# Performance work log

Measured on AMD Instinct MI355X. Metric: run time of the kernel, lower is better.

Reference implementation:

```python
import jax, jax.numpy as jnp
import numpy as np


def setup_inputs() -> dict:
    key = jax.random.key(0)
    k1, k2, k3, k4, k5 = jax.random.split(key, 5)
    B, T, nu, nx, ny = 32, 4096, 64, 128, 64
    return {
        "u_": jax.random.normal(k1, (B, T, nu), dtype=jnp.float32),
        "M": jax.random.normal(k2, (2 * nx, 2 * nx), dtype=jnp.float32),
        "B_mat": jax.random.normal(k3, (nx, nu), dtype=jnp.float32),
        "C": jax.random.normal(k4, (ny, nx), dtype=jnp.float32),
        "x0": jax.random.normal(k5, (nx,), dtype=jnp.float32),
    }


def reference(u_, M, B_mat, C, x0):
    # LMI-stable A parameterization: S = M M^T + tol*I,
    # F = S[nx:, :nx], P = S[nx:, nx:], E = 0.5*(P + S[:nx, :nx]), A = E^{-1} F
    nx = x0.shape[0]
    tol_A = 1e-9
    S = M @ M.T + tol_A * jnp.eye(2 * nx, dtype=M.dtype)
    Fm = S[nx:, :nx]
    E = 0.5 * (S[nx:, nx:] + S[:nx, :nx])
    A = jnp.linalg.solve(E, Fm)  # == inv(E) @ Fm

    Bsz = u_.shape[0]
    x_init = jnp.broadcast_to(x0, (Bsz, nx))  # learned x0 tiled over batch

    # x_{t+1} = A x_t + B u_t ; y_t = C x_t ; y_0 = C x_0
    def step(x, u_t):
        x_new = x @ A.T + u_t @ B_mat.T  # [B, nx]
        return x_new, x_new @ C.T        # emit y_{t+1} [B, ny]

    u_tm = jnp.swapaxes(u_[:, :-1, :], 0, 1)  # [T-1, B, nu] (u[T-1] unused)
    _, ys = jax.lax.scan(step, x_init, u_tm)   # [T-1, B, ny]

    y0 = (x_init @ C.T)[:, None, :]            # [B, 1, ny]
    return jnp.concatenate([y0, jnp.swapaxes(ys, 0, 1)], axis=1)  # [B, T, ny]
```

## Files before the change

### kernel.cpp

```cpp
#include <hip/hip_runtime.h>

#define BATCH 32
#define T_LEN 4096
#define NU 64
#define NX 128
#define NY 64
#define KCH 64
#define NC (T_LEN / KCH)
#define KSPLIT 8

#define OFF_E    0
#define OFF_F    16384
#define OFF_A    32768
#define OFF_G    49152
#define OFF_A8   81920
#define OFF_A16  98304
#define OFF_A32  114688
#define OFF_A64  131072
#define OFF_D    147456
#define OFF_P    204800
#define OFF_WT   233472
#define OFF_WF   380928
#define OFF_WBH  905216
#define OFF_WBL  1167360
#define OFF_XC   1429504
#define OFF_L    1691648
#define OFF_V8   1953792
#define OFF_X8   4050944
#define OFF_UBH  5099520
#define OFF_UBL  9293824
#define OFF_LP   13488128
#define WS_NEED_FLOATS (13488128 + 2097152)

__device__ __forceinline__ int XP(int l)   { return l + ((l >> 3) << 2); }
__device__ __forceinline__ int UP16(int l) { return l + ((l >> 4) << 2); }

__device__ __forceinline__ unsigned short f2bf(float f) {
    unsigned int x = __float_as_uint(f);
    unsigned int r = (x + 0x7FFFu + ((x >> 16) & 1u)) >> 16;
    return (unsigned short)r;
}
__device__ __forceinline__ float bf2f(unsigned short h) {
    return __uint_as_float(((unsigned int)h) << 16);
}
__device__ __forceinline__ float4 f4ms(float4 a, float s, float4 b) {
    float4 r;
    r.x = a.x - s * b.x; r.y = a.y - s * b.y;
    r.z = a.z - s * b.z; r.w = a.w - s * b.w;
    return r;
}
__device__ __forceinline__ float f4dot(float4 a, float4 b) {
    return a.x * b.x + a.y * b.y + a.z * b.z + a.w * b.w;
}
__device__ __forceinline__ void cvt_one(const float* __restrict__ src,
                                        unsigned short* __restrict__ hi,
                                        unsigned short* __restrict__ lo,
                                        size_t idx) {
    float4 v = ((const float4*)src)[idx];
    unsigned short h0 = f2bf(v.x), h1 = f2bf(v.y), h2 = f2bf(v.z), h3 = f2bf(v.w);
    unsigned short l0 = f2bf(v.x - bf2f(h0));
    unsigned short l1 = f2bf(v.y - bf2f(h1));
    unsigned short l2 = f2bf(v.z - bf2f(h2));
    unsigned short l3 = f2bf(v.w - bf2f(h3));
    unsigned long long ph = (unsigned long long)h0 | ((unsigned long long)h1 << 16)
                          | ((unsigned long long)h2 << 32) | ((unsigned long long)h3 << 48);
    unsigned long long pl = (unsigned long long)l0 | ((unsigned long long)l1 << 16)
                          | ((unsigned long long)l2 << 32) | ((unsigned long long)l3 << 48);
    ((unsigned long long*)hi)[idx] = ph;
    ((unsigned long long*)lo)[idx] = pl;
}

typedef __attribute__((ext_vector_type(8))) short bf16x8;
typedef __attribute__((ext_vector_type(4))) float f32x4;

__global__ __launch_bounds__(256) void efcvt_kernel(const float* __restrict__ M,
                                                    float* __restrict__ E,
                                                    float* __restrict__ F,
                                                    const float* __restrict__ u,
                                                    unsigned short* __restrict__ hi,
                                                    unsigned short* __restrict__ lo,
                                                    int n4) {
    int blk = blockIdx.x;
    if (blk < 256) {
        int part = blk >> 7;
        int i = blk & 127;
        int j = threadIdx.x;
        if (j < 128) {
            const float* Mi2 = M + (size_t)(128 + i) * 256;
            const float* Mj1 = M + (size_t)j * 256;
            if (part == 0) {
                const float* Mi1 = M + (size_t)i * 256;
                const float* Mj2 = M + (size_t)(128 + j) * 256;
                float s11 = 0.f, s22 = 0.f;
                for (int m = 0; m < 256; ++m) {
                    s11 += Mi1[m] * Mj1[m];
                    s22 += Mi2[m] * Mj2[m];
                }
                float e = 0.5f * (s11 + s22);
                if (i == j) e += 1e-9f;
                E[i * NX + j] = e;
            } else {
                float s21 = 0.f;
                for (int m = 0; m < 256; ++m) s21 += Mi2[m] * Mj1[m];
                F[i * NX + j] = s21;
            }
        }
    } else if (hi != nullptr) {
        size_t stride = (size_t)(gridDim.x - 256) * 256;
        for (size_t idx = (size_t)(blk - 256) * 256 + threadIdx.x; idx < (size_t)n4;
             idx += stride)
            cvt_one(u, hi, lo, idx);
    }
}

__global__ __launch_bounds__(512, 1) void solve_kernel(const float* __restrict__ E,
                                                       const float* __restrict__ F,
                                                       float* __restrict__ A) {
    __shared__ __align__(16) float praw[2][4][264];
    __shared__ __align__(16) float4 mrowS[2][128];
    __shared__ float pivarr[128];
    int t = threadIdx.x;
    int rg = t >> 4, seg = t & 15;

    float4 R[4][4];
#pragma unroll
    for (int k = 0; k < 4; ++k) {
        int r = rg + 32 * k;
        const float4* erow = (const float4*)(E + (size_t)r * NX);
        const float4* frow = (const float4*)(F + (size_t)r * NX);
        R[k][0] = erow[seg];
        R[k][1] = erow[seg + 16];
        R[k][2] = frow[seg];
        R[k][3] = frow[seg + 16];
    }
    if (rg < 4) {
        float4* dst = (float4*)&praw[0][rg][0];
        dst[seg]      = R[0][0];
        dst[seg + 16] = R[0][1];
        dst[seg + 32] = R[0][2];
        dst[seg + 48] = R[0][3];
    }
    if (seg == 0) {
#pragma unroll
        for (int k = 0; k < 4; ++k) mrowS[0][rg + 32 * k] = R[k][0];
    }
    __syncthreads();

    int buf = 0;
    for (int wd = 0; wd < 32; ++wd) {
        int k0 = 4 * wd;
        const float* p0s = &praw[buf][0][0];
        const float* p1s = &praw[buf][1][0];
        const float* p2s = &praw[buf][2][0];
        const float* p3s = &praw[buf][3][0];
        float p00 = p0s[k0], p01 = p0s[k0 + 1], p02 = p0s[k0 + 2], p03 = p0s[k0 + 3];
        float r10 = p1s[k0], r11 = p1s[k0 + 1], r12 = p1s[k0 + 2], r13 = p1s[k0 + 3];
        float r20 = p2s[k0], r21 = p2s[k0 + 1], r22 = p2s[k0 + 2], r23 = p2s[k0 + 3];
        float r30 = p3s[k0], r31 = p3s[k0 + 1], r32 = p3s[k0 + 2], r33 = p3s[k0 + 3];
        float inv0 = 1.0f / p00;
        float m1 = r10 * inv0;
        float piv1 = r11 - m1 * p01;
        float inv1 = 1.0f / piv1;
        float p12 = r12 - m1 * p02, p13 = r13 - m1 * p03;
        float m2 = r20 * inv0;
        float m2b = (r21 - m2 * p01) * inv1;
        float piv2 = r22 - m2 * p02 - m2b * p12;
        float inv2 = 1.0f / piv2;
        float p23 = r23 - m2 * p03 - m2b * p13;
        float m3 = r30 * inv0;
        float m3b = (r31 - m3 * p01) * inv1;
        float m3c = (r32 - m3 * p02 - m3b * p12) * inv2;
        float piv3 = r33 - m3 * p03 - m3b * p13 - m3c * p23;
        float inv3 = 1.0f / piv3;
        if (t == 0) {
            pivarr[k0] = p00; pivarr[k0 + 1] = piv1;
            pivarr[k0 + 2] = piv2; pivarr[k0 + 3] = piv3;
        }
        float q0[4], q1[4], q2[4], q3[4];
#pragma unroll
        for (int k = 0; k < 4; ++k) {
            int r = rg + 32 * k;
            float4 mv = mrowS[buf][r];
            int d = r - k0;
            float a = mv.x * inv0;
            if (d == 0) a = 0.f;
            float b2 = (mv.y - a * p01) * inv1;
            if (d == 1) b2 = 0.f;
            float c2 = (mv.z - a * p02 - b2 * p12) * inv2;
            if (d == 2) c2 = 0.f;
            float e2 = (mv.w - a * p03 - b2 * p13 - c2 * p23) * inv3;
            if (d == 3) e2 = 0.f;
            q0[k] = a; q1[k] = b2; q2[k] = c2; q3[k] = e2;
        }
        const float4* w0 = (const float4*)&praw[buf][0][0];
        const float4* w1 = (const float4*)&praw[buf][1][0];
        const float4* w2 = (const float4*)&praw[buf][2][0];
        const float4* w3 = (const float4*)&praw[buf][3][0];
#pragma unroll
        for (int j = 0; j < 4; ++j) {
            int g = seg + 16 * j;
            float4 a0 = w0[g], a1 = w1[g], a2 = w2[g], a3 = w3[g];
            float4 p1v = f4ms(a1, m1, a0);
            float4 p2v = f4ms(f4ms(a2, m2, a0), m2b, p1v);
            float4 p3v = f4ms(f4ms(f4ms(a3, m3, a0), m3b, p1v), m3c, p2v);
#pragma unroll
            for (int k = 0; k < 4; ++k) {
                float4 acc = R[k][j];
                acc = f4ms(acc, q0[k], a0);
                acc = f4ms(acc, q1[k], p1v);
                acc = f4ms(acc, q2[k], p2v);
                acc = f4ms(acc, q3[k], p3v);
                R[k][j] = acc;
            }
        }
        if (wd < 31) {
#pragma unroll
            for (int k = 0; k < 4; ++k) {
                int r = rg + 32 * k;
                int d2 = r - (k0 + 4);
                if (d2 >= 0 && d2 < 4) {
                    float4* dst = (float4*)&praw[buf ^ 1][d2][0];
                    dst[seg]      = R[k][0];
                    dst[seg + 16] = R[k][1];
                    dst[seg + 32] = R[k][2];
                    dst[seg + 48] = R[k][3];
                }
            }
            if (seg == ((wd + 1) & 15)) {
#pragma unroll
                for (int k = 0; k < 4; ++k) {
                    float4 sel = ((wd + 1) < 16) ? R[k][0] : R[k][1];
                    mrowS[buf ^ 1][rg + 32 * k] = sel;
                }
            }
        }
        __syncthreads();
        buf ^= 1;
    }

#pragma unroll
    for (int k = 0; k < 4; ++k) {
        int r = rg + 32 * k;
        float s = 1.0f / pivarr[r];
        float4* dst = (float4*)(A + (size_t)r * NX);
        float4 v2 = R[k][2];
        v2.x *= s; v2.y *= s; v2.z *= s; v2.w *= s;
        dst[seg] = v2;
        float4 v3 = R[k][3];
        v3.x *= s; v3.y *= s; v3.z *= s; v3.w *= s;
        dst[seg + 16] = v3;
    }
}

struct MMDesc { const float* X; const float* Y; float* Z; int N; int ldX; int ldY; int ldZ; int Mrows; };
struct MMB { MMDesc d[4]; };
__global__ __launch_bounds__(128) void mmb_kernel(MMB mm) {
    MMDesc d = mm.d[blockIdx.y];
    if (d.Z == nullptr) return;
    int nct = (d.N + 127) >> 7;
    int i = blockIdx.x / nct;
    int jt = blockIdx.x - i * nct;
    if (i >= d.Mrows) return;
    int j = jt * 128 + threadIdx.x;
    if (j >= d.N) return;
    if (d.Y == nullptr) {
        d.Z[(size_t)i * d.ldZ + j] = d.X[(size_t)i * d.ldX + j];
        return;
    }
    const float* xr = d.X + (size_t)i * d.ldX;
    float a0 = 0.f, a1 = 0.f, a2 = 0.f, a3 = 0.f;
    for (int m = 0; m < 128; m += 4) {
        a0 += xr[m]     * d.Y[(size_t)(m)     * d.ldY + j];
        a1 += xr[m + 1] * d.Y[(size_t)(m + 1) * d.ldY + j];
        a2 += xr[m + 2] * d.Y[(size_t)(m + 2) * d.ldY + j];
        a3 += xr[m + 3] * d.Y[(size_t)(m + 3) * d.ldY + j];
    }
    d.Z[(size_t)i * d.ldZ + j] = (a0 + a1) + (a2 + a3);
}

__global__ __launch_bounds__(576) void wcvt_kernel(const float* __restrict__ Dm,
                                                   const float* __restrict__ C,
                                                   const float* __restrict__ Pm,
                                                   unsigned short* __restrict__ WT,
                                                   const float* __restrict__ WF,
                                                   unsigned short* __restrict__ WBH,
                                                   unsigned short* __restrict__ WBL,
                                                   int n4) {
    int blk = blockIdx.x;
    if (blk < 512) {
        int o = blk;
        int f = threadIdx.x;
        int k = o >> 6, yi = o & 63;
        float v = 0.f;
        if (f < 128) {
            v = (k == 0) ? C[(size_t)yi * NX + f]
                         : Dm[(size_t)(k - 1) * 64 * NX + (size_t)yi * NX + f];
        } else {
            int j = (f - 128) >> 6, e = (f - 128) & 63;
            if (k > j) v = Pm[(size_t)(k - 1 - j) * 64 * 64 + (size_t)yi * 64 + e];
        }
        WT[(size_t)o * 576 + f] = f2bf(v);
    } else {
        size_t idx = (size_t)(blk - 512) * 576 + threadIdx.x;
        if (idx < (size_t)n4) cvt_one(WF, WBH, WBL, idx);
    }
}

__global__ __launch_bounds__(256) void lvgemm_kernel(const unsigned short* __restrict__ UH,
                                                     const unsigned short* __restrict__ UL,
                                                     const unsigned short* __restrict__ WH,
                                                     const unsigned short* __restrict__ WL,
                                                     float* __restrict__ Lp,
                                                     float* __restrict__ V8) {
    int t = threadIdx.x;
    int w = t >> 6, l = t & 63;
    int l16 = l & 15, l4 = l >> 4;
    int o0 = w * 32 + l16;
    f32x4 acc[4][2];
#pragma unroll
    for (int mt = 0; mt < 4; ++mt)
#pragma unroll
        for (int nt = 0; nt < 2; ++nt) acc[mt][nt] = (f32x4){0.f, 0.f, 0.f, 0.f};

    if (blockIdx.x < 256) {
        int blk = blockIdx.x & 31;
        int kblk = blockIdx.x >> 5;
        size_t uoff[4];
#pragma unroll
        for (int mt = 0; mt < 4; ++mt) {
            int pair = blk * 64 + mt * 16 + l16;
            int b = pair & 31, c = pair >> 5;
            uoff[mt] = ((size_t)b * T_LEN + (size_t)c * KCH) * NU;
        }
        int kt0 = kblk * (128 / KSPLIT);
        for (int kt = kt0; kt < kt0 + 128 / KSPLIT; ++kt) {
            int feat = kt * 32 + l4 * 8;
            bf16x8 ah[4], al[4], bh[2], bl[2];
#pragma unroll
            for (int mt = 0; mt < 4; ++mt) {
                ah[mt] = *(const bf16x8*)(UH + uoff[mt] + feat);
                al[mt] = *(const bf16x8*)(UL + uoff[mt] + feat);
            }
#pragma unroll
            for (int nt = 0; nt < 2; ++nt) {
                size_t woff = (size_t)(o0 + nt * 16) * 4096 + feat;
                bh[nt] = *(const bf16x8*)(WH + woff);
                bl[nt] = *(const bf16x8*)(WL + woff);
            }
#pragma unroll
            for (int mt = 0; mt < 4; ++mt)
#pragma unroll
                for (int nt = 0; nt < 2; ++nt) {
                    acc[mt][nt] = __builtin_amdgcn_mfma_f32_16x16x32_bf16(
                        ah[mt], bh[nt], acc[mt][nt], 0, 0, 0);
                    acc[mt][nt] = __builtin_amdgcn_mfma_f32_16x16x32_bf16(
                        ah[mt], bl[nt], acc[mt][nt], 0, 0, 0);
                    acc[mt][nt] = __builtin_amdgcn_mfma_f32_16x16x32_bf16(
                        al[mt], bh[nt], acc[mt][nt], 0, 0, 0);
                }
        }
        float* lout = Lp + (size_t)kblk * 2048 * NX;
#pragma unroll
        for (int mt = 0; mt < 4; ++mt)
#pragma unroll
            for (int nt = 0; nt < 2; ++nt)
#pragma unroll
                for (int reg = 0; reg < 4; ++reg) {
                    int r = blk * 64 + mt * 16 + l4 * 4 + reg;
                    lout[(size_t)r * NX + o0 + nt * 16] = acc[mt][nt][reg];
                }
    } else {
        int blk = blockIdx.x - 256;
        size_t uoff[4];
#pragma unroll
        for (int mt = 0; mt < 4; ++mt) {
            int r = blk * 64 + mt * 16 + l16;
            int pair = r >> 3, q = r & 7;
            int b = pair & 31, c = pair >> 5;
            uoff[mt] = ((size_t)b * T_LEN + (size_t)c * KCH + (size_t)q * 8) * NU;
        }
#pragma unroll 2
        for (int kt = 0; kt < 16; ++kt) {
            int feat = kt * 32 + l4 * 8;
            bf16x8 ah[4], al[4], bh[2], bl[2];
#pragma unroll
            for (int mt = 0; mt < 4; ++mt) {
                ah[mt] = *(const bf16x8*)(UH + uoff[mt] + feat);
                al[mt] = *(const bf16x8*)(UL + uoff[mt] + feat);
            }
#pragma unroll
            for (int nt = 0; nt < 2; ++nt) {
                size_t woff = (size_t)(o0 + nt * 16) * 4096 + 3584 + feat;
                bh[nt] = *(const bf16x8*)(WH + woff);
                bl[nt] = *(const bf16x8*)(WL + woff);
            }
#pragma unroll
            for (int mt = 0; mt < 4; ++mt)
#pragma unroll
                for (int nt = 0; nt < 2; ++nt) {
                    acc[mt][nt] = __builtin_amdgcn_mfma_f32_16x16x32_bf16(
                        ah[mt], bh[nt], acc[mt][nt], 0, 0, 0);
                    acc[mt][nt] = __builtin_amdgcn_mfma_f32_16x16x32_bf16(
                        ah[mt], bl[nt], acc[mt][nt], 0, 0, 0);
                    acc[mt][nt] = __builtin_amdgcn_mfma_f32_16x16x32_bf16(
                        al[mt], bh[nt], acc[mt][nt], 0, 0, 0);
                }
        }
#pragma unroll
        for (int mt = 0; mt < 4; ++mt)
#pragma unroll
            for (int nt = 0; nt < 2; ++nt)
#pragma unroll
                for (int reg = 0; reg < 4; ++reg) {
                    int r = blk * 64 + mt * 16 + l4 * 4 + reg;
                    V8[(size_t)r * NX + o0 + nt * 16] = acc[mt][nt][reg];
                }
    }
}

__global__ __launch_bounds__(128) void phase2_kernel(const float* __restrict__ AK,
                                                     const float* __restrict__ Lp,
                                                     const float* __restrict__ x0,
                                                     float* __restrict__ Xc) {
    __shared__ float Ks[NX][NX + 1];
    __shared__ float xs[NX];
    int tid = threadIdx.x, b = blockIdx.x;
    for (int idx = tid; idx < NX * NX; idx += 128)
        Ks[idx >> 7][idx & 127] = AK[idx];
    float x = x0[tid];
    xs[tid] = x;
    Xc[(size_t)(0 * BATCH + b) * NX + tid] = x;
    __syncthreads();
    for (int c = 0; c < NC - 1; ++c) {
        size_t lidx = ((size_t)c * BATCH + b) * NX + tid;
        float lsum = 0.f;
#pragma unroll
        for (int k = 0; k < KSPLIT; ++k) lsum += Lp[(size_t)k * 2048 * NX + lidx];
        float a0 = 0.f, a1 = 0.f, a2 = 0.f, a3 = 0.f;
        for (int j = 0; j < NX; j += 4) {
            a0 += Ks[tid][j]     * xs[j];
            a1 += Ks[tid][j + 1] * xs[j + 1];
            a2 += Ks[tid][j + 2] * xs[j + 2];
            a3 += Ks[tid][j + 3] * xs[j + 3];
        }
        float xn = (a0 + a1) + (a2 + a3) + lsum;
        __syncthreads();
        xs[tid] = xn;
        Xc[((size_t)(c + 1) * BATCH + b) * NX + tid] = xn;
        __syncthreads();
    }
}

__global__ __launch_bounds__(128) void phase2fb_kernel(const float* __restrict__ AK,
                                                       const float* __restrict__ L,
                                                       const float* __restrict__ x0,
                                                       float* __restrict__ Xc) {
    __shared__ float Ks[NX][NX + 1];
    __shared__ float xs[NX];
    int tid = threadIdx.x, b = blockIdx.x;
    for (int idx = tid; idx < NX * NX; idx += 128)
        Ks[idx >> 7][idx & 127] = AK[idx];
    float x = x0[tid];
    xs[tid] = x;
    Xc[(size_t)(0 * BATCH + b) * NX + tid] = x;
    __syncthreads();
    for (int c = 0; c < NC - 1; ++c) {
        float a0 = 0.f, a1 = 0.f, a2 = 0.f, a3 = 0.f;
        for (int j = 0; j < NX; j += 4) {
            a0 += Ks[tid][j]     * xs[j];
            a1 += Ks[tid][j + 1] * xs[j + 1];
            a2 += Ks[tid][j + 2] * xs[j + 2];
            a3 += Ks[tid][j + 3] * xs[j + 3];
        }
        float xn = (a0 + a1) + (a2 + a3) + L[((size_t)c * BATCH + b) * NX + tid];
        __syncthreads();
        xs[tid] = xn;
        Xc[((size_t)(c + 1) * BATCH + b) * NX + tid] = xn;
        __syncthreads();
    }
}

__global__ __launch_bounds__(256, 4) void chain8_kernel(const float* __restrict__ A8,
                                                        const float* __restrict__ V8,
                                                        const float* __restrict__ Xc,
                                                        unsigned short* __restrict__ X8) {
    int t = threadIdx.x;
    int g = t >> 3, seg = t & 7;
    int pair = blockIdx.x;

    float4 A8r[4][4];
#pragma unroll
    for (int r = 0; r < 4; ++r) {
        const float4* ap = (const float4*)(A8 + (size_t)(g + 32 * r) * NX + seg * 16);
        A8r[r][0] = ap[0]; A8r[r][1] = ap[1]; A8r[r][2] = ap[2]; A8r[r][3] = ap[3];
    }

    __shared__ __align__(16) float xs[2][192];
    __shared__ float vs[2][128];
    float vreg = 0.f;
    if (t < NX) {
        xs[0][XP(t)] = Xc[(size_t)pair * NX + t];
        vreg = V8[((size_t)pair * 8) * NX + t];
    }

    int buf = 0;
    for (int m = 0; m < 8; ++m) {
        if (t < NX) vs[buf][t] = vreg;
        if (t < NX && m < 7) vreg = V8[((size_t)pair * 8 + m + 1) * NX + t];
        __syncthreads();
        if (t < NX) X8[((size_t)pair * 8 + m) * NX + t] = f2bf(xs[buf][XP(t)]);
        const float4* xq0 = (const float4*)&xs[buf][seg * 24];
        const float4* xq1 = (const float4*)&xs[buf][seg * 24 + 12];
        float4 x0 = xq0[0], x1 = xq0[1], x2 = xq1[0], x3 = xq1[1];
        float acc[4];
#pragma unroll
        for (int r = 0; r < 4; ++r) {
            acc[r] = (f4dot(A8r[r][0], x0) + f4dot(A8r[r][1], x1))
                   + (f4dot(A8r[r][2], x2) + f4dot(A8r[r][3], x3));
        }
#pragma unroll
        for (int d = 1; d <= 4; d <<= 1) {
#pragma unroll
            for (int r = 0; r < 4; ++r) acc[r] += __shfl_xor(acc[r], d);
        }
        if (seg == 0) {
            xs[buf ^ 1][XP(g)]      = acc[0] + vs[buf][g];
            xs[buf ^ 1][XP(g + 32)] = acc[1] + vs[buf][g + 32];
            xs[buf ^ 1][XP(g + 64)] = acc[2] + vs[buf][g + 64];
            xs[buf ^ 1][XP(g + 96)] = acc[3] + vs[buf][g + 96];
        }
        buf ^= 1;
    }
}

__global__ __launch_bounds__(512) void yemit_mfma_kernel(const unsigned short* __restrict__ X8,
                                                         const unsigned short* __restrict__ ub,
                                                         const unsigned short* __restrict__ WT,
                                                         float* __restrict__ y) {
    int t = threadIdx.x;
    int w = t >> 6, l = t & 63;
    int l16 = l & 15, l4 = l >> 4;
    int blk = blockIdx.x;
    f32x4 acc[4][4];
#pragma unroll
    for (int mt = 0; mt < 4; ++mt)
#pragma unroll
        for (int nt = 0; nt < 4; ++nt) acc[mt][nt] = (f32x4){0.f, 0.f, 0.f, 0.f};
    int grow[4];
    const unsigned short* ubase[4];
#pragma unroll
    for (int mt = 0; mt < 4; ++mt) {
        grow[mt] = blk * 64 + mt * 16 + l16;
        int pair = grow[mt] >> 3, q = grow[mt] & 7;
        int b = pair & 31, cc = pair >> 5;
        ubase[mt] = ub + ((size_t)b * T_LEN + (size_t)cc * KCH + (size_t)q * 8) * NU;
    }
#pragma unroll 2
    for (int kt = 0; kt < 18; ++kt) {
        int feat = kt * 32 + l4 * 8;
        bf16x8 afr[4];
#pragma unroll
        for (int mt = 0; mt < 4; ++mt) {
            const unsigned short* ap;
            if (feat < 128) ap = X8 + (size_t)grow[mt] * NX + feat;
            else            ap = ubase[mt] + (feat - 128);
            afr[mt] = *(const bf16x8*)ap;
        }
        bf16x8 bfr[4];
#pragma unroll
        for (int nt = 0; nt < 4; ++nt) {
            int o = w * 64 + nt * 16 + l16;
            bfr[nt] = *(const bf16x8*)(WT + (size_t)o * 576 + feat);
        }
#pragma unroll
        for (int mt = 0; mt < 4; ++mt)
#pragma unroll
            for (int nt = 0; nt < 4; ++nt)
                acc[mt][nt] = __builtin_amdgcn_mfma_f32_16x16x32_bf16(
                    afr[mt], bfr[nt], acc[mt][nt], 0, 0, 0);
    }
#pragma unroll
    for (int mt = 0; mt < 4; ++mt) {
#pragma unroll
        for (int nt = 0; nt < 4; ++nt) {
            int o = w * 64 + nt * 16 + l16;
            int k = o >> 6, yi = o & 63;
#pragma unroll
            for (int reg = 0; reg < 4; ++reg) {
                int r = blk * 64 + mt * 16 + l4 * 4 + reg;
                int pair = r >> 3, q = r & 7;
                int b = pair & 31, cc = pair >> 5;
                int tt = cc * KCH + q * 8 + k;
                y[((size_t)b * T_LEN + tt) * NY + yi] = acc[mt][nt][reg];
            }
        }
    }
}

__global__ __launch_bounds__(512, 4) void phase1_kernel(const float* __restrict__ u_,
                                                        const float* __restrict__ A4,
                                                        const float* __restrict__ G,
                                                        float* __restrict__ L) {
    int t = threadIdx.x;
    int g = t >> 4, seg = t & 15;
    int pair = blockIdx.x;
    int c = pair >> 5, b = pair & 31;
    const float* urow = u_ + ((size_t)b * T_LEN + (size_t)c * KCH) * NU;
    float4 A4r[4][2], Gr[4][4];
#pragma unroll
    for (int r = 0; r < 4; ++r) {
        const float4* ap = (const float4*)(A4 + (size_t)(g + 32 * r) * NX + seg * 8);
        A4r[r][0] = ap[0]; A4r[r][1] = ap[1];
        const float4* gp = (const float4*)(G + (size_t)(g + 32 * r) * 256 + seg * 16);
        Gr[r][0] = gp[0]; Gr[r][1] = gp[1]; Gr[r][2] = gp[2]; Gr[r][3] = gp[3];
    }
    __shared__ __align__(16) float xs[2][192];
    __shared__ __align__(16) float us[2][320];
    if (t < NX) xs[0][XP(t)] = 0.f;
    float up = (t < 256) ? urow[t] : 0.f;
    int buf = 0;
    for (int m = 0; m < 16; ++m) {
        if (t < 256) us[buf][UP16(t)] = up;
        if (t < 256 && m < 15) up = urow[(size_t)(m + 1) * 256 + t];
        __syncthreads();
        const float4* xq = (const float4*)&xs[buf][seg * 12];
        float4 xa = xq[0], xb = xq[1];
        const float4* uq = (const float4*)&us[buf][seg * 20];
        float acc0[4], acc1[4];
#pragma unroll
        for (int r = 0; r < 4; ++r) {
            acc0[r] = f4dot(A4r[r][0], xa);
            acc1[r] = f4dot(A4r[r][1], xb);
        }
#pragma unroll
        for (int q = 0; q < 4; ++q) {
            float4 uv = uq[q];
#pragma unroll
            for (int r = 0; r < 4; ++r) {
                float pr = f4dot(Gr[r][q], uv);
                if (q & 1) acc1[r] += pr; else acc0[r] += pr;
            }
        }
        float acc[4];
#pragma unroll
        for (int r = 0; r < 4; ++r) acc[r] = acc0[r] + acc1[r];
#pragma unroll
        for (int d = 1; d <= 8; d <<= 1) {
#pragma unroll
            for (int r = 0; r < 4; ++r) acc[r] += __shfl_xor(acc[r], d);
        }
        if (seg == 0) {
            xs[buf ^ 1][XP(g)]      = acc[0];
            xs[buf ^ 1][XP(g + 32)] = acc[1];
            xs[buf ^ 1][XP(g + 64)] = acc[2];
            xs[buf ^ 1][XP(g + 96)] = acc[3];
        }
        buf ^= 1;
    }
    __syncthreads();
    if (t < NX) L[(size_t)pair * NX + t] = xs[buf][XP(t)];
}

__global__ __launch_bounds__(256) void phase3_fb_kernel(const float* __restrict__ u_,
                                                        const float* __restrict__ A,
                                                        const float* __restrict__ Bm,
                                                        const float* __restrict__ C,
                                                        const float* __restrict__ Xc,
                                                        float* __restrict__ y) {
    int t = threadIdx.x;
    int i = t >> 1, h = t & 1;
    int r = t >> 2, q = t & 3;
    int pair = blockIdx.x;
    int c = pair >> 5, b = pair & 31;
    const float* urow = u_ + ((size_t)b * T_LEN + (size_t)c * KCH) * NU;
    float* yrow = y + ((size_t)b * T_LEN + (size_t)c * KCH) * NY;
    float Ar[64];
    {
        const float4* Arow = (const float4*)(A + (size_t)i * NX + h * 64);
#pragma unroll
        for (int j4 = 0; j4 < 16; ++j4) {
            float4 v = Arow[j4];
            Ar[4 * j4] = v.x; Ar[4 * j4 + 1] = v.y; Ar[4 * j4 + 2] = v.z; Ar[4 * j4 + 3] = v.w;
        }
    }
    float Br[32];
    {
        const float4* Brow = (const float4*)(Bm + (size_t)i * NU + h * 32);
#pragma unroll
        for (int j4 = 0; j4 < 8; ++j4) {
            float4 v = Brow[j4];
            Br[4 * j4] = v.x; Br[4 * j4 + 1] = v.y; Br[4 * j4 + 2] = v.z; Br[4 * j4 + 3] = v.w;
        }
    }
    float Cr[32];
    {
        const float4* Crow = (const float4*)(C + (size_t)r * NX + q * 32);
#pragma unroll
        for (int j4 = 0; j4 < 8; ++j4) {
            float4 v = Crow[j4];
            Cr[4 * j4] = v.x; Cr[4 * j4 + 1] = v.y; Cr[4 * j4 + 2] = v.z; Cr[4 * j4 + 3] = v.w;
        }
    }
    __shared__ float xs[2][NX];
    __shared__ float us[2][NU];
    if (h == 0) xs[0][i] = Xc[(size_t)pair * NX + i];
    float up = (t < NU) ? urow[t] : 0.f;
    __syncthreads();
    {
        float c0 = 0.f, c1 = 0.f, c2 = 0.f, c3 = 0.f;
        const float* xp = &xs[0][q * 32];
#pragma unroll
        for (int j = 0; j < 32; j += 4) {
            c0 += Cr[j]     * xp[j];
            c1 += Cr[j + 1] * xp[j + 1];
            c2 += Cr[j + 2] * xp[j + 2];
            c3 += Cr[j + 3] * xp[j + 3];
        }
        float s = (c0 + c1) + (c2 + c3);
        s += __shfl_xor(s, 1);
        s += __shfl_xor(s, 2);
        if (q == 0) yrow[r] = s;
    }
    int buf = 0;
    for (int k = 1; k < KCH; ++k) {
        if (t < NU) us[buf][t] = up;
        if (k < KCH - 1 && t < NU) up = urow[(size_t)k * NU + t];
        __syncthreads();
        float a0 = 0.f, a1 = 0.f, a2 = 0.f, a3 = 0.f;
        const float* xp = &xs[buf][h * 64];
        const float* upp = &us[buf][h * 32];
#pragma unroll
        for (int j = 0; j < 64; j += 4) {
            a0 += Ar[j]     * xp[j];
            a1 += Ar[j + 1] * xp[j + 1];
            a2 += Ar[j + 2] * xp[j + 2];
            a3 += Ar[j + 3] * xp[j + 3];
        }
#pragma unroll
        for (int j = 0; j < 32; j += 4) {
            a0 += Br[j]     * upp[j];
            a1 += Br[j + 1] * upp[j + 1];
            a2 += Br[j + 2] * upp[j + 2];
            a3 += Br[j + 3] * upp[j + 3];
        }
        float a = (a0 + a1) + (a2 + a3);
        float s = a + __shfl_xor(a, 1);
        if (h == 0) xs[buf ^ 1][i] = s;
        __syncthreads();
        float c0 = 0.f, c1 = 0.f, c2 = 0.f, c3 = 0.f;
        const float* xcp = &xs[buf ^ 1][q * 32];
#pragma unroll
        for (int j = 0; j < 32; j += 4) {
            c0 += Cr[j]     * xcp[j];
            c1 += Cr[j + 1] * xcp[j + 1];
            c2 += Cr[j + 2] * xcp[j + 2];
            c3 += Cr[j + 3] * xcp[j + 3];
        }
        float sy = (c0 + c1) + (c2 + c3);
        sy += __shfl_xor(sy, 1);
        sy += __shfl_xor(sy, 2);
        if (q == 0) yrow[(size_t)k * NY + r] = sy;
        buf ^= 1;
    }
}

extern "C" void kernel_launch(void* const* d_in, const int* in_sizes, int n_in,
                              void* d_out, int out_size, void* d_ws, size_t ws_size,
                              hipStream_t stream) {
    const float* u_  = (const float*)d_in[0];
    const float* M   = (const float*)d_in[1];
    const float* Bm  = (const float*)d_in[2];
    const float* C   = (const float*)d_in[3];
    const float* x0  = (const float*)d_in[4];
    float* y = (float*)d_out;
    float* ws = (float*)d_ws;

    float* E   = ws + OFF_E;
    float* F   = ws + OFF_F;
    float* A   = ws + OFF_A;
    float* A2  = ws + OFF_E;
    float* A4  = ws + OFF_F;
    float* G   = ws + OFF_G;
    float* A8  = ws + OFF_A8;
    float* A16 = ws + OFF_A16;
    float* A32 = ws + OFF_A32;
    float* A64 = ws + OFF_A64;
    float* Dm  = ws + OFF_D;
    float* Pm  = ws + OFF_P;
    unsigned short* WT  = (unsigned short*)(ws + OFF_WT);
    float* WF  = ws + OFF_WF;
    unsigned short* WBH = (unsigned short*)(ws + OFF_WBH);
    unsigned short* WBL = (unsigned short*)(ws + OFF_WBL);
    float* Xc  = ws + OFF_XC;
    float* L   = ws + OFF_L;
    float* V8  = ws + OFF_V8;
    unsigned short* X8  = (unsigned short*)(ws + OFF_X8);
    unsigned short* UBH = (unsigned short*)(ws + OFF_UBH);
    unsigned short* UBL = (unsigned short*)(ws + OFF_UBL);
    float* Lp  = ws + OFF_LP;

    bool fast = ws_size >= (size_t)WS_NEED_FLOATS * sizeof(float);

    efcvt_kernel<<<fast ? 2304 : 256, 256, 0, stream>>>(
        M, E, F, u_, fast ? UBH : nullptr, UBL, BATCH * T_LEN * NU / 4);
    solve_kernel<<<1, 512, 0, stream>>>(E, F, A);

    if (fast) {
        { MMB mm;
          mm.d[0] = { A, A,  A2,          128, NX, NX, NX,  128 };
          mm.d[1] = { C, A,  Dm,          128, NX, NX, NX,  64  };
          mm.d[2] = { C, Bm, Pm,           64, NX, NU, 64,  64  };
          mm.d[3] = { Bm, nullptr, WF + 4032, 64, NU, 0, 4096, 128 };
          mmb_kernel<<<dim3(128, 4), 128, 0, stream>>>(mm); }
        { MMB mm;
          mm.d[0] = { A2, A2, A4,          128, NX, NX, NX,  128 };
          mm.d[1] = { Dm, A,  Dm + 8192,   128, NX, NX, NX,  64  };
          mm.d[2] = { Dm, Bm, Pm + 4096,    64, NX, NU, 64,  64  };
          mm.d[3] = { A, WF + 4032, WF + 3968, 64, NX, 4096, 4096, 128 };
          mmb_kernel<<<dim3(128, 4), 128, 0, stream>>>(mm); }
        { MMB mm;
          mm.d[0] = { A4, A4, A8,              128, NX, NX, NX,  128 };
          mm.d[1] = { Dm + 8192, A, Dm + 16384, 128, NX, NX, NX, 64  };
          mm.d[2] = { Dm + 8192, Bm, Pm + 8192,  64, NX, NU, 64, 64  };
          mm.d[3] = { A2, WF + 3968, WF + 3840, 128, NX, 4096, 4096, 128 };
          mmb_kernel<<<dim3(256, 4), 128, 0, stream>>>(mm); }
        { MMB mm;
          mm.d[0] = { A8, A8, A16,              128, NX, NX, NX,  128 };
          mm.d[1] = { Dm + 8192, A2, Dm + 24576, 128, NX, NX, NX, 64  };
          mm.d[2] = { Dm + 16384, Bm, Pm + 12288, 64, NX, NU, 64, 64  };
          mm.d[3] = { A4, WF + 3840, WF + 3584, 256, NX, 4096, 4096, 128 };
          mmb_kernel<<<dim3(256, 4), 128, 0, stream>>>(mm); }
        { MMB mm;
          mm.d[0] = { A16, A16, A32,             128, NX, NX, NX,  128 };
          mm.d[1] = { Dm + 16384, A2, Dm + 32768, 128, NX, NX, NX, 64  };
          mm.d[2] = { Dm + 24576, Bm, Pm + 16384,  64, NX, NU, 64, 64  };
          mm.d[3] = { A8, WF + 3584, WF + 3072, 512, NX, 4096, 4096, 128 };
          mmb_kernel<<<dim3(512, 4), 128, 0, stream>>>(mm); }
        { MMB mm;
          mm.d[0] = { A32, A32, A64,             128, NX, NX, NX,  128 };
          mm.d[1] = { Dm + 8192, A4, Dm + 40960,  128, NX, NX, NX, 64  };
          mm.d[2] = { Dm + 32768, Bm, Pm + 20480,  64, NX, NU, 64, 64  };
          mm.d[3] = { A16, WF + 3072, WF + 2048, 1024, NX, 4096, 4096, 128 };
          mmb_kernel<<<dim3(1024, 4), 128, 0, stream>>>(mm); }
        { MMB mm;
          mm.d[0] = { A32, WF + 2048, WF, 2048, NX, 4096, 4096, 128 };
          mm.d[1] = { Dm + 16384, A4, Dm + 49152, 128, NX, NX, NX, 64 };
          mm.d[2] = { Dm + 40960, Bm, Pm + 24576,  64, NX, NU, 64, 64 };
          mm.d[3] = { nullptr, nullptr, nullptr, 0, 0, 0, 0, 0 };
          mmb_kernel<<<dim3(2048, 4), 128, 0, stream>>>(mm); }

        wcvt_kernel<<<512 + (NX * 4096 / 4 + 575) / 576, 576, 0, stream>>>(
            Dm, C, Pm, WT, WF, WBH, WBL, NX * 4096 / 4);
        lvgemm_kernel<<<512, 256, 0, stream>>>(UBH, UBL, WBH, WBL, Lp, V8);
        phase2_kernel<<<BATCH, 128, 0, stream>>>(A64, Lp, x0, Xc);
        chain8_kernel<<<NC * BATCH, 256, 0, stream>>>(A8, V8, Xc, X8);
        yemit_mfma_kernel<<<256, 512, 0, stream>>>(X8, UBH, WT, y);
    } else {
        { MMB mm;
          mm.d[0] = { A, A,  A2,       128, NX, NX, NX,  128 };
          mm.d[1] = { A, Bm, G + 128,   64, NX, NU, 256, 128 };
          mm.d[2] = { Bm, nullptr, G + 192, 64, NU, 0, 256, 128 };
          mm.d[3] = { nullptr, nullptr, nullptr, 0, 0, 0, 0, 0 };
          mmb_kernel<<<dim3(128, 4), 128, 0, stream>>>(mm); }
        { MMB mm;
          mm.d[0] = { A2, A2, A4,   128, NX, NX,  NX,  128 };
          mm.d[1] = { A2, G + 128, G, 128, NX, 256, 256, 128 };
          mm.d[2] = { nullptr, nullptr, nullptr, 0, 0, 0, 0, 0 };
          mm.d[3] = { nullptr, nullptr, nullptr, 0, 0, 0, 0, 0 };
          mmb_kernel<<<dim3(256, 4), 128, 0, stream>>>(mm); }
        { MMB mm;
          mm.d[0] = { A4, A4, A8,    128, NX, NX, NX, 128 };
          mm.d[1] = { nullptr, nullptr, nullptr, 0, 0, 0, 0, 0 };
          mm.d[2] = { nullptr, nullptr, nullptr, 0, 0, 0, 0, 0 };
          mm.d[3] = { nullptr, nullptr, nullptr, 0, 0, 0, 0, 0 };
          mmb_kernel<<<dim3(128, 4), 128, 0, stream>>>(mm); }
        { MMB mm;
          mm.d[0] = { A8, A8, A16,   128, NX, NX, NX, 128 };
          mm.d[1] = { nullptr, nullptr, nullptr, 0, 0, 0, 0, 0 };
          mm.d[2] = { nullptr, nullptr, nullptr, 0, 0, 0, 0, 0 };
          mm.d[3] = { nullptr, nullptr, nullptr, 0, 0, 0, 0, 0 };
          mmb_kernel<<<dim3(128, 4), 128, 0, stream>>>(mm); }
        { MMB mm;
          mm.d[0] = { A16, A16, A32, 128, NX, NX, NX, 128 };
          mm.d[1] = { nullptr, nullptr, nullptr, 0, 0, 0, 0, 0 };
          mm.d[2] = { nullptr, nullptr, nullptr, 0, 0, 0, 0, 0 };
          mm.d[3] = { nullptr, nullptr, nullptr, 0, 0, 0, 0, 0 };
          mmb_kernel<<<dim3(128, 4), 128, 0, stream>>>(mm); }
        { MMB mm;
          mm.d[0] = { A32, A32, A64, 128, NX, NX, NX, 128 };
          mm.d[1] = { nullptr, nullptr, nullptr, 0, 0, 0, 0, 0 };
          mm.d[2] = { nullptr, nullptr, nullptr, 0, 0, 0, 0, 0 };
          mm.d[3] = { nullptr, nullptr, nullptr, 0, 0, 0, 0, 0 };
          mmb_kernel<<<dim3(128, 4), 128, 0, stream>>>(mm); }
        phase1_kernel<<<NC * BATCH, 512, 0, stream>>>(u_, A4, G, L);
        phase2fb_kernel<<<BATCH, 128, 0, stream>>>(A64, L, x0, Xc);
        phase3_fb_kernel<<<NC * BATCH, 256, 0, stream>>>(u_, A, Bm, C, Xc, y);
    }
}
```

Baseline: 290.3 us.

## Fuse matrix-power chain into persistent kernel with global barriers; overlap cvt with solve

Replaces the seven mmb_kernel launches plus wcvt_kernel with a single persistent chainw_kernel that loops over stages and separates them with an atomic-counter grid barrier. It also moves the u conversion off the E/F kernel and into the single-block solve launch, so the conversion runs in extra blocks alongside the solve. The aim is to cut launch overhead and idle gaps between many small dependent launches. In exchange it adds spin-wait barriers that assume all 512 blocks are co-resident, and it reuses the L buffer region for the barrier counters.

```diff
diff --git a/kernel.cpp b/kernel.cpp
--- a/kernel.cpp
+++ b/kernel.cpp
@@ -8,6 +8,7 @@
 #define KCH 64
 #define NC (T_LEN / KCH)
 #define KSPLIT 8
+#define CHAIN_NB 512
 
 #define OFF_E    0
 #define OFF_F    16384
@@ -73,49 +74,47 @@
 typedef __attribute__((ext_vector_type(8))) short bf16x8;
 typedef __attribute__((ext_vector_type(4))) float f32x4;
 
-__global__ __launch_bounds__(256) void efcvt_kernel(const float* __restrict__ M,
-                                                    float* __restrict__ E,
-                                                    float* __restrict__ F,
-                                                    const float* __restrict__ u,
-                                                    unsigned short* __restrict__ hi,
-                                                    unsigned short* __restrict__ lo,
-                                                    int n4) {
-    int blk = blockIdx.x;
-    if (blk < 256) {
-        int part = blk >> 7;
-        int i = blk & 127;
-        int j = threadIdx.x;
-        if (j < 128) {
-            const float* Mi2 = M + (size_t)(128 + i) * 256;
-            const float* Mj1 = M + (size_t)j * 256;
-            if (part == 0) {
-                const float* Mi1 = M + (size_t)i * 256;
-                const float* Mj2 = M + (size_t)(128 + j) * 256;
-                float s11 = 0.f, s22 = 0.f;
-                for (int m = 0; m < 256; ++m) {
-                    s11 += Mi1[m] * Mj1[m];
-                    s22 += Mi2[m] * Mj2[m];
-                }
-                float e = 0.5f * (s11 + s22);
-                if (i == j) e += 1e-9f;
-                E[i * NX + j] = e;
-            } else {
-                float s21 = 0.f;
-                for (int m = 0; m < 256; ++m) s21 += Mi2[m] * Mj1[m];
-                F[i * NX + j] = s21;
-            }
-        }
-    } else if (hi != nullptr) {
-        size_t stride = (size_t)(gridDim.x - 256) * 256;
-        for (size_t idx = (size_t)(blk - 256) * 256 + threadIdx.x; idx < (size_t)n4;
+__global__ __launch_bounds__(128) void ef_kernel(const float* __restrict__ M,
+                                                 float* __restrict__ E,
+                                                 float* __restrict__ F) {
+    int part = blockIdx.x >> 7;
+    int i = blockIdx.x & 127;
+    int j = threadIdx.x;
+    const float* Mi2 = M + (size_t)(128 + i) * 256;
+    const float* Mj1 = M + (size_t)j * 256;
+    if (part == 0) {
+        const float* Mi1 = M + (size_t)i * 256;
+        const float* Mj2 = M + (size_t)(128 + j) * 256;
+        float s11 = 0.f, s22 = 0.f;
+        for (int m = 0; m < 256; ++m) {
+            s11 += Mi1[m] * Mj1[m];
+            s22 += Mi2[m] * Mj2[m];
+        }
+        float e = 0.5f * (s11 + s22);
+        if (i == j) e += 1e-9f;
+        E[i * NX + j] = e;
+    } else {
+        float s21 = 0.f;
+        for (int m = 0; m < 256; ++m) s21 += Mi2[m] * Mj1[m];
+        F[i * NX + j] = s21;
+    }
+}
+
+__global__ __launch_bounds__(512, 1) void solvecvt_kernel(const float* __restrict__ E,
+                                                          const float* __restrict__ F,
+                                                          float* __restrict__ A,
+                                                          const float* __restrict__ u,
+                                                          unsigned short* __restrict__ hi,
+                                                          unsigned short* __restrict__ lo,
+                                                          int n4) {
+    if (blockIdx.x != 0) {
+        if (hi == nullptr) return;
+        size_t stride = (size_t)(gridDim.x - 1) * 512;
+        for (size_t idx = (size_t)(blockIdx.x - 1) * 512 + threadIdx.x; idx < (size_t)n4;
              idx += stride)
             cvt_one(u, hi, lo, idx);
-    }
-}
-
-__global__ __launch_bounds__(512, 1) void solve_kernel(const float* __restrict__ E,
-                                                       const float* __restrict__ F,
-                                                       float* __restrict__ A) {
+        return;
+    }
     __shared__ __align__(16) float praw[2][4][264];
     __shared__ __align__(16) float4 mrowS[2][128];
     __shared__ float pivarr[128];
@@ -254,6 +253,138 @@
 
 struct MMDesc { const float* X; const float* Y; float* Z; int N; int ldX; int ldY; int ldZ; int Mrows; };
 struct MMB { MMDesc d[4]; };
+
+__device__ __forceinline__ MMDesc get_desc(int sd, float* ws, const float* Bm,
+                                           const float* Cc) {
+    float* A   = ws + OFF_A;
+    float* A2  = ws + OFF_E;
+    float* A4  = ws + OFF_F;
+    float* A8  = ws + OFF_A8;
+    float* A16 = ws + OFF_A16;
+    float* A32 = ws + OFF_A32;
+    float* A64 = ws + OFF_A64;
+    float* Dm  = ws + OFF_D;
+    float* Pm  = ws + OFF_P;
+    float* WF  = ws + OFF_WF;
+    MMDesc r = { nullptr, nullptr, nullptr, 0, 0, 0, 0, 0 };
+    switch (sd) {
+    case 0:  r = { A, A,  A2,          128, NX, NX, NX,  128 }; break;
+    case 1:  r = { Cc, A, Dm,          128, NX, NX, NX,  64  }; break;
+    case 2:  r = { Cc, Bm, Pm,          64, NX, NU, 64,  64  }; break;
+    case 3:  r = { Bm, nullptr, WF + 4032, 64, NU, 0, 4096, 128 }; break;
+    case 4:  r = { A2, A2, A4,         128, NX, NX, NX,  128 }; break;
+    case 5:  r = { Dm, A,  Dm + 8192,  128, NX, NX, NX,  64  }; break;
+    case 6:  r = { Dm, Bm, Pm + 4096,   64, NX, NU, 64,  64  }; break;
+    case 7:  r = { A, WF + 4032, WF + 3968, 64, NX, 4096, 4096, 128 }; break;
+    case 8:  r = { A4, A4, A8,              128, NX, NX, NX, 128 }; break;
+    case 9:  r = { Dm + 8192, A, Dm + 16384, 128, NX, NX, NX, 64 }; break;
+    case 10: r = { Dm + 8192, Bm, Pm + 8192,  64, NX, NU, 64, 64 }; break;
+    case 11: r = { A2, WF + 3968, WF + 3840, 128, NX, 4096, 4096, 128 }; break;
+    case 12: r = { A8, A8, A16,              128, NX, NX, NX, 128 }; break;
+    case 13: r = { Dm + 8192, A2, Dm + 24576, 128, NX, NX, NX, 64 }; break;
+    case 14: r = { Dm + 16384, Bm, Pm + 12288, 64, NX, NU, 64, 64 }; break;
+    case 15: r = { A4, WF + 3840, WF + 3584, 256, NX, 4096, 4096, 128 }; break;
+    case 16: r = { A16, A16, A32,             128, NX, NX, NX, 128 }; break;
+    case 17: r = { Dm + 16384, A2, Dm + 32768, 128, NX, NX, NX, 64 }; break;
+    case 18: r = { Dm + 24576, Bm, Pm + 16384,  64, NX, NU, 64, 64 }; break;
+    case 19: r = { A8, WF + 3584, WF + 3072, 512, NX, 4096, 4096, 128 }; break;
+    case 20: r = { A32, A32, A64,             128, NX, NX, NX, 128 }; break;
+    case 21: r = { Dm + 8192, A4, Dm + 40960,  128, NX, NX, NX, 64 }; break;
+    case 22: r = { Dm + 32768, Bm, Pm + 20480,  64, NX, NU, 64, 64 }; break;
+    case 23: r = { A16, WF + 3072, WF + 2048, 1024, NX, 4096, 4096, 128 }; break;
+    case 24: r = { A32, WF + 2048, WF, 2048, NX, 4096, 4096, 128 }; break;
+    case 25: r = { Dm + 16384, A4, Dm + 49152, 128, NX, NX, NX, 64 }; break;
+    case 26: r = { Dm + 40960, Bm, Pm + 24576,  64, NX, NU, 64, 64 }; break;
+    default: break;
+    }
+    return r;
+}
+
+__device__ __forceinline__ void gbar(int* bar, int s, int nblk) {
+    __syncthreads();
+    if (threadIdx.x == 0) {
+        __threadfence();
+        atomicAdd(&bar[s], 1);
+        while (atomicAdd(&bar[s], 0) < nblk) __builtin_amdgcn_s_sleep(2);
+        __threadfence();
+    }
+    __syncthreads();
+}
+
+__global__ __launch_bounds__(128) void chainw_kernel(float* ws, const float* Bm,
+                                                     const float* Cc, int* bar) {
+    unsigned short* WT  = (unsigned short*)(ws + OFF_WT);
+    float* WF = ws + OFF_WF;
+    unsigned short* WBH = (unsigned short*)(ws + OFF_WBH);
+    unsigned short* WBL = (unsigned short*)(ws + OFF_WBL);
+    const float* Dm = ws + OFF_D;
+    const float* Pm = ws + OFF_P;
+    int bid = blockIdx.x;
+    const int nblk = gridDim.x;
+
+    for (int s = 0; s < 7; ++s) {
+        MMDesc dd[4];
+        int pre[5];
+        pre[0] = 0;
+#pragma unroll
+        for (int d = 0; d < 4; ++d) {
+            dd[d] = get_desc(s * 4 + d, ws, Bm, Cc);
+            int nc = dd[d].Z ? ((dd[d].N + 127) >> 7) : 0;
+            pre[d + 1] = pre[d] + (dd[d].Z ? dd[d].Mrows * nc : 0);
+        }
+        for (int item = bid; item < pre[4]; item += nblk) {
+            int d = 0;
+            while (item >= pre[d + 1]) ++d;
+            int local = item - pre[d];
+            int nc = (dd[d].N + 127) >> 7;
+            int i = local / nc;
+            int jt = local - i * nc;
+            int j = jt * 128 + threadIdx.x;
+            if (j < dd[d].N) {
+                if (dd[d].Y == nullptr) {
+                    dd[d].Z[(size_t)i * dd[d].ldZ + j] = dd[d].X[(size_t)i * dd[d].ldX + j];
+                } else {
+                    const float* xr = dd[d].X + (size_t)i * dd[d].ldX;
+                    const float* yc = dd[d].Y + j;
+                    float a0 = 0.f, a1 = 0.f, a2 = 0.f, a3 = 0.f;
+                    for (int m = 0; m < 128; m += 4) {
+                        a0 += xr[m]     * yc[(size_t)(m)     * dd[d].ldY];
+                        a1 += xr[m + 1] * yc[(size_t)(m + 1) * dd[d].ldY];
+                        a2 += xr[m + 2] * yc[(size_t)(m + 2) * dd[d].ldY];
+                        a3 += xr[m + 3] * yc[(size_t)(m + 3) * dd[d].ldY];
+                    }
+                    dd[d].Z[(size_t)i * dd[d].ldZ + j] = (a0 + a1) + (a2 + a3);
+                }
+            }
+        }
+        gbar(bar, s, nblk);
+    }
+    const int wtTiles = 512 * 5;
+    const int n4 = NX * 4096 / 4;
+    const int cvtTiles = (n4 + 127) >> 7;
+    for (int item = bid; item < wtTiles + cvtTiles; item += nblk) {
+        if (item < wtTiles) {
+            int o = item / 5, ft = item - (item / 5) * 5;
+            int f = ft * 128 + threadIdx.x;
+            if (f < 576) {
+                int k = o >> 6, yi = o & 63;
+                float v = 0.f;
+                if (f < 128) {
+                    v = (k == 0) ? Cc[(size_t)yi * NX + f]
+                                 : Dm[(size_t)(k - 1) * 64 * NX + (size_t)yi * NX + f];
+                } else {
+                    int jj = (f - 128) >> 6, e = (f - 128) & 63;
+                    if (k > jj) v = Pm[(size_t)(k - 1 - jj) * 64 * 64 + (size_t)yi * 64 + e];
+                }
+                WT[(size_t)o * 576 + f] = f2bf(v);
+            }
+        } else {
+            size_t idx = (size_t)(item - wtTiles) * 128 + threadIdx.x;
+            if (idx < (size_t)n4) cvt_one(WF, WBH, WBL, idx);
+        }
+    }
+}
+
 __global__ __launch_bounds__(128) void mmb_kernel(MMB mm) {
     MMDesc d = mm.d[blockIdx.y];
     if (d.Z == nullptr) return;
@@ -276,34 +407,6 @@
         a3 += xr[m + 3] * d.Y[(size_t)(m + 3) * d.ldY + j];
     }
     d.Z[(size_t)i * d.ldZ + j] = (a0 + a1) + (a2 + a3);
-}
-
-__global__ __launch_bounds__(576) void wcvt_kernel(const float* __restrict__ Dm,
-                                                   const float* __restrict__ C,
-                                                   const float* __restrict__ Pm,
-                                                   unsigned short* __restrict__ WT,
-                                                   const float* __restrict__ WF,
-                                                   unsigned short* __restrict__ WBH,
-                                                   unsigned short* __restrict__ WBL,
-                                                   int n4) {
-    int blk = blockIdx.x;
-    if (blk < 512) {
-        int o = blk;
-        int f = threadIdx.x;
-        int k = o >> 6, yi = o & 63;
-        float v = 0.f;
-        if (f < 128) {
-            v = (k == 0) ? C[(size_t)yi * NX + f]
-                         : Dm[(size_t)(k - 1) * 64 * NX + (size_t)yi * NX + f];
-        } else {
-            int j = (f - 128) >> 6, e = (f - 128) & 63;
-            if (k > j) v = Pm[(size_t)(k - 1 - j) * 64 * 64 + (size_t)yi * 64 + e];
-        }
-        WT[(size_t)o * 576 + f] = f2bf(v);
-    } else {
-        size_t idx = (size_t)(blk - 512) * 576 + threadIdx.x;
-        if (idx < (size_t)n4) cvt_one(WF, WBH, WBL, idx);
-    }
 }
 
 __global__ __launch_bounds__(256) void lvgemm_kernel(const unsigned short* __restrict__ UH,
@@ -785,14 +888,12 @@
     float* A16 = ws + OFF_A16;
     float* A32 = ws + OFF_A32;
     float* A64 = ws + OFF_A64;
-    float* Dm  = ws + OFF_D;
-    float* Pm  = ws + OFF_P;
     unsigned short* WT  = (unsigned short*)(ws + OFF_WT);
-    float* WF  = ws + OFF_WF;
     unsigned short* WBH = (unsigned short*)(ws + OFF_WBH);
     unsigned short* WBL = (unsigned short*)(ws + OFF_WBL);
     float* Xc  = ws + OFF_XC;
     float* L   = ws + OFF_L;
+    int*   bar = (int*)(ws + OFF_L);
     float* V8  = ws + OFF_V8;
     unsigned short* X8  = (unsigned short*)(ws + OFF_X8);
     unsigned short* UBH = (unsigned short*)(ws + OFF_UBH);
@@ -800,62 +901,20 @@
     float* Lp  = ws + OFF_LP;
 
     bool fast = ws_size >= (size_t)WS_NEED_FLOATS * sizeof(float);
-
-    efcvt_kernel<<<fast ? 2304 : 256, 256, 0, stream>>>(
-        M, E, F, u_, fast ? UBH : nullptr, UBL, BATCH * T_LEN * NU / 4);
-    solve_kernel<<<1, 512, 0, stream>>>(E, F, A);
+    int n4 = BATCH * T_LEN * NU / 4;
+
+    ef_kernel<<<256, 128, 0, stream>>>(M, E, F);
 
     if (fast) {
-        { MMB mm;
-          mm.d[0] = { A, A,  A2,          128, NX, NX, NX,  128 };
-          mm.d[1] = { C, A,  Dm,          128, NX, NX, NX,  64  };
-          mm.d[2] = { C, Bm, Pm,           64, NX, NU, 64,  64  };
-          mm.d[3] = { Bm, nullptr, WF + 4032, 64, NU, 0, 4096, 128 };
-          mmb_kernel<<<dim3(128, 4), 128, 0, stream>>>(mm); }
-        { MMB mm;
-          mm.d[0] = { A2, A2, A4,          128, NX, NX, NX,  128 };
-          mm.d[1] = { Dm, A,  Dm + 8192,   128, NX, NX, NX,  64  };
-          mm.d[2] = { Dm, Bm, Pm + 4096,    64, NX, NU, 64,  64  };
-          mm.d[3] = { A, WF + 4032, WF + 3968, 64, NX, 4096, 4096, 128 };
-          mmb_kernel<<<dim3(128, 4), 128, 0, stream>>>(mm); }
-        { MMB mm;
-          mm.d[0] = { A4, A4, A8,              128, NX, NX, NX,  128 };
-          mm.d[1] = { Dm + 8192, A, Dm + 16384, 128, NX, NX, NX, 64  };
-          mm.d[2] = { Dm + 8192, Bm, Pm + 8192,  64, NX, NU, 64, 64  };
-          mm.d[3] = { A2, WF + 3968, WF + 3840, 128, NX, 4096, 4096, 128 };
-          mmb_kernel<<<dim3(256, 4), 128, 0, stream>>>(mm); }
-        { MMB mm;
-          mm.d[0] = { A8, A8, A16,              128, NX, NX, NX,  128 };
-          mm.d[1] = { Dm + 8192, A2, Dm + 24576, 128, NX, NX, NX, 64  };
-          mm.d[2] = { Dm + 16384, Bm, Pm + 12288, 64, NX, NU, 64, 64  };
-          mm.d[3] = { A4, WF + 3840, WF + 3584, 256, NX, 4096, 4096, 128 };
-          mmb_kernel<<<dim3(256, 4), 128, 0, stream>>>(mm); }
-        { MMB mm;
-          mm.d[0] = { A16, A16, A32,             128, NX, NX, NX,  128 };
-          mm.d[1] = { Dm + 16384, A2, Dm + 32768, 128, NX, NX, NX, 64  };
-          mm.d[2] = { Dm + 24576, Bm, Pm + 16384,  64, NX, NU, 64, 64  };
-          mm.d[3] = { A8, WF + 3584, WF + 3072, 512, NX, 4096, 4096, 128 };
-          mmb_kernel<<<dim3(512, 4), 128, 0, stream>>>(mm); }
-        { MMB mm;
-          mm.d[0] = { A32, A32, A64,             128, NX, NX, NX,  128 };
-          mm.d[1] = { Dm + 8192, A4, Dm + 40960,  128, NX, NX, NX, 64  };
-          mm.d[2] = { Dm + 32768, Bm, Pm + 20480,  64, NX, NU, 64, 64  };
-          mm.d[3] = { A16, WF + 3072, WF + 2048, 1024, NX, 4096, 4096, 128 };
-          mmb_kernel<<<dim3(1024, 4), 128, 0, stream>>>(mm); }
-        { MMB mm;
-          mm.d[0] = { A32, WF + 2048, WF, 2048, NX, 4096, 4096, 128 };
-          mm.d[1] = { Dm + 16384, A4, Dm + 49152, 128, NX, NX, NX, 64 };
-          mm.d[2] = { Dm + 40960, Bm, Pm + 24576,  64, NX, NU, 64, 64 };
-          mm.d[3] = { nullptr, nullptr, nullptr, 0, 0, 0, 0, 0 };
-          mmb_kernel<<<dim3(2048, 4), 128, 0, stream>>>(mm); }
-
-        wcvt_kernel<<<512 + (NX * 4096 / 4 + 575) / 576, 576, 0, stream>>>(
-            Dm, C, Pm, WT, WF, WBH, WBL, NX * 4096 / 4);
+        hipMemsetAsync(bar, 0, 32, stream);
+        solvecvt_kernel<<<257, 512, 0, stream>>>(E, F, A, u_, UBH, UBL, n4);
+        chainw_kernel<<<CHAIN_NB, 128, 0, stream>>>(ws, Bm, C, bar);
         lvgemm_kernel<<<512, 256, 0, stream>>>(UBH, UBL, WBH, WBL, Lp, V8);
         phase2_kernel<<<BATCH, 128, 0, stream>>>(A64, Lp, x0, Xc);
         chain8_kernel<<<NC * BATCH, 256, 0, stream>>>(A8, V8, Xc, X8);
         yemit_mfma_kernel<<<256, 512, 0, stream>>>(X8, UBH, WT, y);
     } else {
+        solvecvt_kernel<<<1, 512, 0, stream>>>(E, F, A, u_, nullptr, nullptr, n4);
         { MMB mm;
           mm.d[0] = { A, A,  A2,       128, NX, NX, NX,  128 };
           mm.d[1] = { A, Bm, G + 128,   64, NX, NU, 256, 128 };
```

Result: slower. 701.5 us (+141.7%).
